# Optimization experiments

Measured on AMD Instinct MI355X. Metric: run time of the kernel, lower is better.

Reference implementation:

```python
import jax, jax.numpy as jnp
import numpy as np
from jax import lax

KERNEL = 15
IGNORE = 255


def setup_inputs() -> dict:
    key = jax.random.key(0)
    k1, k2 = jax.random.split(key)
    B, C, H, W = 32, 2, 480, 864
    logits = jax.random.normal(k1, (B, C, H, W), dtype=jnp.float32)
    labels = jax.random.randint(k2, (B, H, W), 0, 2, dtype=jnp.int32)
    return {"logits": logits, "labels": labels}


def _boundary_edgemap(labels):
    # labels: [B, H, W] int32 with values in {0, 1, IGNORE}
    lbl = labels.astype(jnp.int32)
    # np_label = label*255, with ignore pixels set to 0 (matches cv2 path)
    np_label = jnp.where(lbl == IGNORE, 0, lbl * 255)
    win = (1, KERNEL, KERNEL)
    strides = (1, 1, 1)
    # cv2.erode with ones kernel == 15x15 min filter (border value +inf -> pad 255)
    erosion = lax.reduce_window(np_label, jnp.int32(255), lax.min, win, strides, "SAME")
    # cv2.dilate == 15x15 max filter (border value -inf -> pad 0)
    dilation = lax.reduce_window(np_label, jnp.int32(0), lax.max, win, strides, "SAME")
    boundary = dilation - erosion  # >0 exactly on the morphological boundary band
    edgemap = jnp.where(boundary > 0, lbl, IGNORE)
    edgemap = jnp.where(lbl == IGNORE, IGNORE, edgemap)
    return edgemap


def reference(logits, labels):
    # logits: [B, C, H, W] log-probabilities, labels: [B, H, W]
    edgemap = _boundary_edgemap(labels)  # [B, H, W]
    valid = edgemap != IGNORE
    tgt = jnp.where(valid, edgemap, 0)  # safe index for ignored pixels
    # gather logits[b, tgt, h, w] -> [B, H, W]
    picked = jnp.take_along_axis(logits, tgt[:, None, :, :], axis=1)[:, 0]
    # NLLLoss with ignore_index: mean of -logp over valid pixels
    n_valid = jnp.maximum(jnp.sum(valid), 1)
    loss = -jnp.sum(jnp.where(valid, picked, 0.0)) / n_valid.astype(logits.dtype)
    return loss
```

## Files before the change

kernel.cpp:

```cpp
#include <hip/hip_runtime.h>


namespace {
constexpr int B_ = 32;
constexpr int H_ = 480;
constexpr int W_ = 864;
constexpr int NW = 27;
constexpr int NMASK = B_ * H_ * NW;
constexpr int SROWS = 50;
constexpr int NSTRIP = 10;
constexpr int NWAVE_M = B_ * NW * NSTRIP;
constexpr int NBLK_M = NWAVE_M / 4;
constexpr int NF4 = B_ * 2 * H_ * W_ / 4;
constexpr int NBLK_G = NF4 / 1024;
constexpr int NWAVE_G = NBLK_G * 4;
constexpr size_t OFF_IGN  = 2u << 20;
constexpr size_t OFF_VAL  = 4u << 20;
constexpr size_t OFF_CNT  = 6u << 20;
constexpr size_t OFF_SUM  = 7u << 20;
}

extern "C" __global__ __launch_bounds__(256)
void bl_bitpack(const int* __restrict__ labels,
                unsigned* __restrict__ Am, unsigned* __restrict__ Im)
{
  const int t = blockIdx.x * 256 + threadIdx.x;
  const int4* p = (const int4*)(labels + (size_t)t * 32);
  unsigned a = 0, ig = 0;
#pragma unroll
  for (int k = 0; k < 8; ++k) {
    const int4 v = p[k];
    a  |= ((v.x == 1)   ? 1u : 0u) << (4 * k) | ((v.y == 1)   ? 2u : 0u) << (4 * k)
       |  ((v.z == 1)   ? 4u : 0u) << (4 * k) | ((v.w == 1)   ? 8u : 0u) << (4 * k);
    ig |= ((v.x == 255) ? 1u : 0u) << (4 * k) | ((v.y == 255) ? 2u : 0u) << (4 * k)
       |  ((v.z == 255) ? 4u : 0u) << (4 * k) | ((v.w == 255) ? 8u : 0u) << (4 * k);
  }
  Am[t] = a;
  Im[t] = ig;
}

__device__ __forceinline__ unsigned hwin(unsigned w0, unsigned w1, unsigned w2) {
  unsigned long long L = ((unsigned long long)w1 << 32) | w0;
  unsigned long long R = ((unsigned long long)w2 << 32) | w1;
  L |= L << 1; L |= L << 2; L |= L << 4;
  R |= R >> 1; R |= R >> 2; R |= R >> 4;
  return (unsigned)(L >> 32) | (unsigned)R;
}

__device__ __forceinline__ unsigned vwin(unsigned x) {
  unsigned u = x, d = x;
  u |= __shfl_up(u, 1, 64);  u |= __shfl_up(u, 2, 64);  u |= __shfl_up(u, 4, 64);
  d |= __shfl_down(d, 1, 64); d |= __shfl_down(d, 2, 64); d |= __shfl_down(d, 4, 64);
  return u | d;
}

extern "C" __global__ __launch_bounds__(256)
void bl_morph(const unsigned* __restrict__ Am, const unsigned* __restrict__ Im,
              unsigned* __restrict__ Vm, float* __restrict__ cnt_part)
{
  const int tid = threadIdx.x;
  const int lane = tid & 63;
  const int wid = blockIdx.x * 4 + (tid >> 6);
  const int b = wid / (NW * NSTRIP);
  const int rem = wid - b * (NW * NSTRIP);
  const int dc = rem / NSTRIP;
  const int s = rem - dc * NSTRIP;

  const int gr = SROWS * s - 7 + lane;
  const bool inrow = (gr >= 0) && (gr < H_);
  const bool out_lane = (lane >= 7) && (lane <= 56) && (gr < H_);

  unsigned A0 = 0, A1 = 0, A2 = 0, Ic = 0;
  size_t rbase = 0;
  if (inrow) {
    rbase = ((size_t)b * H_ + gr) * NW + dc;
    A1 = Am[rbase];
    Ic = Im[rbase];
    if (dc > 0) A0 = Am[rbase - 1];
    if (dc < NW - 1) A2 = Am[rbase + 1];
  }
  const unsigned N0 = (inrow && dc > 0) ? ~A0 : 0u;
  const unsigned N1 = inrow ? ~A1 : 0u;
  const unsigned N2 = (inrow && dc < NW - 1) ? ~A2 : 0u;

  const unsigned vA = vwin(hwin(A0, A1, A2));
  const unsigned vN = vwin(hwin(N0, N1, N2));
  const unsigned valid = out_lane ? (vA & vN & ~Ic) : 0u;

  if (out_lane) Vm[rbase] = valid;

  unsigned lcnt = __popc(valid);
#pragma unroll
  for (int off = 32; off > 0; off >>= 1) lcnt += __shfl_down(lcnt, off, 64);
  if (lane == 0) cnt_part[wid] = (float)lcnt;
}

extern "C" __global__ __launch_bounds__(256)
void bl_gather(const float* __restrict__ logits,
               const unsigned* __restrict__ Am, const unsigned* __restrict__ Vm,
               float* __restrict__ sum_part)
{
  const int tid = threadIdx.x;
  float lsum = 0.f;
#pragma unroll
  for (int it = 0; it < 4; ++it) {
    const int g = blockIdx.x * 1024 + it * 256 + tid;
    const float4 v = *(const float4*)(logits + (size_t)g * 4);
    const int row = g / 216;
    const int col4 = g - row * 216;
    const int col = col4 * 4;
    const int b = row / 960;
    const int remr = row - b * 960;
    const int c = remr / 480;
    const int h = remr - c * 480;
    const size_t mi = ((size_t)b * H_ + h) * NW + (col >> 5);
    const unsigned vm = Vm[mi];
    const unsigned am = Am[mi];
    const unsigned want = c ? (vm & am) : (vm & ~am);
    const unsigned sel = (want >> (col & 31)) & 0xFu;
    lsum += (sel & 1u) ? v.x : 0.f;
    lsum += (sel & 2u) ? v.y : 0.f;
    lsum += (sel & 4u) ? v.z : 0.f;
    lsum += (sel & 8u) ? v.w : 0.f;
  }
#pragma unroll
  for (int off = 32; off > 0; off >>= 1) lsum += __shfl_down(lsum, off, 64);
  if ((tid & 63) == 0) sum_part[blockIdx.x * 4 + (tid >> 6)] = lsum;
}

extern "C" __global__ __launch_bounds__(1024)
void bl_final(const float* __restrict__ cnt_part,
              const float* __restrict__ sum_part, float* __restrict__ out)
{
  __shared__ double red_s[16];
  __shared__ double red_c[16];
  const int tid = threadIdx.x;
  double s = 0.0, cc = 0.0;
  for (int i = tid; i < NWAVE_G; i += 1024) s += (double)sum_part[i];
  for (int i = tid; i < NWAVE_M; i += 1024) cc += (double)cnt_part[i];
#pragma unroll
  for (int off = 32; off > 0; off >>= 1) {
    s += __shfl_down(s, off, 64);
    cc += __shfl_down(cc, off, 64);
  }
  const int wave = tid >> 6;
  if ((tid & 63) == 0) { red_s[wave] = s; red_c[wave] = cc; }
  __syncthreads();
  if (tid == 0) {
    double ts = 0.0, tc = 0.0;
#pragma unroll
    for (int i = 0; i < 16; ++i) { ts += red_s[i]; tc += red_c[i]; }
    if (tc < 1.0) tc = 1.0;
    out[0] = (float)(-ts / tc);
  }
}

extern "C" void kernel_launch(void* const* d_in, const int* in_sizes, int n_in,
                              void* d_out, int out_size, void* d_ws, size_t ws_size,
                              hipStream_t stream)
{
  const float* logits = (const float*)d_in[0];
  const int* labels = (const int*)d_in[1];
  float* out = (float*)d_out;
  unsigned* Am = (unsigned*)d_ws;
  unsigned* Im = (unsigned*)((char*)d_ws + OFF_IGN);
  unsigned* Vm = (unsigned*)((char*)d_ws + OFF_VAL);
  float* cnt_part = (float*)((char*)d_ws + OFF_CNT);
  float* sum_part = (float*)((char*)d_ws + OFF_SUM);

  bl_bitpack<<<NMASK / 256, 256, 0, stream>>>(labels, Am, Im);
  bl_morph<<<NBLK_M, 256, 0, stream>>>(Am, Im, Vm, cnt_part);
  bl_gather<<<NBLK_G, 256, 0, stream>>>(logits, Am, Vm, sum_part);
  bl_final<<<1, 1024, 0, stream>>>(cnt_part, sum_part, out);
}
```

Before: 211.8 us.

## Coalesce bitpack loads, precompute per-float4 select bytes, nontemporal logits loads

Bitpack now has each lane load one contiguous int4 and merges nibbles across lanes with shuffles, so global loads are coalesced. A new expand kernel turns the valid and label bitmasks into one selector byte per float4 of logits, laid out to match the logits order. The gather kernel then reads a single byte per float4 and drops its index division math, and it loads logits with nontemporal hints. The cost is an extra kernel launch and about 7 MB of extra selector traffic.

```diff
diff --git a/kernel.cpp b/kernel.cpp
--- a/kernel.cpp
+++ b/kernel.cpp
@@ -14,29 +14,41 @@
 constexpr int NF4 = B_ * 2 * H_ * W_ / 4;
 constexpr int NBLK_G = NF4 / 1024;
 constexpr int NWAVE_G = NBLK_G * 4;
-constexpr size_t OFF_IGN  = 2u << 20;
-constexpr size_t OFF_VAL  = 4u << 20;
-constexpr size_t OFF_CNT  = 6u << 20;
-constexpr size_t OFF_SUM  = 7u << 20;
-}
+constexpr int NBLK_P = NMASK / 32;
+constexpr size_t OFF_IM  = 2u << 20;
+constexpr size_t OFF_VM  = 4u << 20;
+constexpr size_t OFF_CNT = 6u << 20;
+constexpr size_t OFF_SEL = 8u << 20;
+constexpr size_t OFF_SUM = 16u << 20;
+}
+
+typedef float f4v __attribute__((ext_vector_type(4)));
 
 extern "C" __global__ __launch_bounds__(256)
 void bl_bitpack(const int* __restrict__ labels,
                 unsigned* __restrict__ Am, unsigned* __restrict__ Im)
 {
-  const int t = blockIdx.x * 256 + threadIdx.x;
-  const int4* p = (const int4*)(labels + (size_t)t * 32);
-  unsigned a = 0, ig = 0;
-#pragma unroll
-  for (int k = 0; k < 8; ++k) {
-    const int4 v = p[k];
-    a  |= ((v.x == 1)   ? 1u : 0u) << (4 * k) | ((v.y == 1)   ? 2u : 0u) << (4 * k)
-       |  ((v.z == 1)   ? 4u : 0u) << (4 * k) | ((v.w == 1)   ? 8u : 0u) << (4 * k);
-    ig |= ((v.x == 255) ? 1u : 0u) << (4 * k) | ((v.y == 255) ? 2u : 0u) << (4 * k)
-       |  ((v.z == 255) ? 4u : 0u) << (4 * k) | ((v.w == 255) ? 8u : 0u) << (4 * k);
-  }
-  Am[t] = a;
-  Im[t] = ig;
+  const int tid = threadIdx.x;
+  const int lane = tid & 63;
+  const int wid = blockIdx.x * 4 + (tid >> 6);
+  const int4 v = *(const int4*)(labels + (size_t)wid * 256 + lane * 4);
+  const unsigned nibA = (v.x == 1 ? 1u : 0u) | (v.y == 1 ? 2u : 0u) |
+                        (v.z == 1 ? 4u : 0u) | (v.w == 1 ? 8u : 0u);
+  const unsigned nibI = (v.x == 255 ? 1u : 0u) | (v.y == 255 ? 2u : 0u) |
+                        (v.z == 255 ? 4u : 0u) | (v.w == 255 ? 8u : 0u);
+  unsigned long long x = (unsigned long long)nibA |
+                         ((unsigned long long)nibI << 32);
+  unsigned long long p = __shfl_xor(x, 1, 64);
+  x = (lane & 1) ? (p | (x << 4)) : (x | (p << 4));
+  p = __shfl_xor(x, 2, 64);
+  x = (lane & 2) ? (p | (x << 8)) : (x | (p << 8));
+  p = __shfl_xor(x, 4, 64);
+  x = (lane & 4) ? (p | (x << 16)) : (x | (p << 16));
+  if ((lane & 7) == 0) {
+    const int di = wid * 8 + (lane >> 3);
+    Am[di] = (unsigned)x;
+    Im[di] = (unsigned)(x >> 32);
+  }
 }
 
 __device__ __forceinline__ unsigned hwin(unsigned w0, unsigned w1, unsigned w2) {
@@ -95,9 +107,33 @@
   if (lane == 0) cnt_part[wid] = (float)lcnt;
 }
 
+__device__ __forceinline__ unsigned long long spread(unsigned w) {
+  unsigned long long x = w;
+  x = (x | (x << 16)) & 0x0000FFFF0000FFFFull;
+  x = (x | (x << 8))  & 0x00FF00FF00FF00FFull;
+  x = (x | (x << 4))  & 0x0F0F0F0F0F0F0F0Full;
+  return x;
+}
+
+extern "C" __global__ __launch_bounds__(256)
+void bl_expand(const unsigned* __restrict__ Am, const unsigned* __restrict__ Vm,
+               unsigned long long* __restrict__ sel8)
+{
+  const int t = blockIdx.x * 256 + threadIdx.x;
+  const unsigned v = Vm[t];
+  const unsigned a = Am[t];
+  const int b = t / (H_ * NW);
+  const int r2 = t - b * (H_ * NW);
+  const int h = r2 / NW;
+  const int dc = r2 - h * NW;
+  const size_t s0 = ((size_t)(b * 2 * H_ + h)) * NW + dc;
+  sel8[s0] = spread(v & ~a);
+  sel8[s0 + (size_t)H_ * NW] = spread(v & a);
+}
+
 extern "C" __global__ __launch_bounds__(256)
 void bl_gather(const float* __restrict__ logits,
-               const unsigned* __restrict__ Am, const unsigned* __restrict__ Vm,
+               const unsigned char* __restrict__ sel,
                float* __restrict__ sum_part)
 {
   const int tid = threadIdx.x;
@@ -105,23 +141,12 @@
 #pragma unroll
   for (int it = 0; it < 4; ++it) {
     const int g = blockIdx.x * 1024 + it * 256 + tid;
-    const float4 v = *(const float4*)(logits + (size_t)g * 4);
-    const int row = g / 216;
-    const int col4 = g - row * 216;
-    const int col = col4 * 4;
-    const int b = row / 960;
-    const int remr = row - b * 960;
-    const int c = remr / 480;
-    const int h = remr - c * 480;
-    const size_t mi = ((size_t)b * H_ + h) * NW + (col >> 5);
-    const unsigned vm = Vm[mi];
-    const unsigned am = Am[mi];
-    const unsigned want = c ? (vm & am) : (vm & ~am);
-    const unsigned sel = (want >> (col & 31)) & 0xFu;
-    lsum += (sel & 1u) ? v.x : 0.f;
-    lsum += (sel & 2u) ? v.y : 0.f;
-    lsum += (sel & 4u) ? v.z : 0.f;
-    lsum += (sel & 8u) ? v.w : 0.f;
+    const f4v v = __builtin_nontemporal_load((const f4v*)(logits + (size_t)g * 4));
+    const unsigned s = sel[g];
+    lsum += (s & 1u) ? v.x : 0.f;
+    lsum += (s & 2u) ? v.y : 0.f;
+    lsum += (s & 4u) ? v.z : 0.f;
+    lsum += (s & 8u) ? v.w : 0.f;
   }
 #pragma unroll
   for (int off = 32; off > 0; off >>= 1) lsum += __shfl_down(lsum, off, 64);
@@ -163,13 +188,15 @@
   const int* labels = (const int*)d_in[1];
   float* out = (float*)d_out;
   unsigned* Am = (unsigned*)d_ws;
-  unsigned* Im = (unsigned*)((char*)d_ws + OFF_IGN);
-  unsigned* Vm = (unsigned*)((char*)d_ws + OFF_VAL);
+  unsigned* Im = (unsigned*)((char*)d_ws + OFF_IM);
+  unsigned* Vm = (unsigned*)((char*)d_ws + OFF_VM);
   float* cnt_part = (float*)((char*)d_ws + OFF_CNT);
+  unsigned long long* sel8 = (unsigned long long*)((char*)d_ws + OFF_SEL);
   float* sum_part = (float*)((char*)d_ws + OFF_SUM);
 
-  bl_bitpack<<<NMASK / 256, 256, 0, stream>>>(labels, Am, Im);
+  bl_bitpack<<<NBLK_P, 256, 0, stream>>>(labels, Am, Im);
   bl_morph<<<NBLK_M, 256, 0, stream>>>(Am, Im, Vm, cnt_part);
-  bl_gather<<<NBLK_G, 256, 0, stream>>>(logits, Am, Vm, sum_part);
+  bl_expand<<<NMASK / 256, 256, 0, stream>>>(Am, Vm, sel8);
+  bl_gather<<<NBLK_G, 256, 0, stream>>>(logits, (const unsigned char*)sel8, sum_part);
   bl_final<<<1, 1024, 0, stream>>>(cnt_part, sum_part, out);
 }
```

New measurement: 206.3 us. -2.6%, faster.
